# Performance work log

Measured on AMD Instinct MI355X. Metric: run time of the kernel, lower is better.

The kernel has to match this reference:

```python
import jax, jax.numpy as jnp
import numpy as np

H, NH, QLORA, KVLORA, DN, DR, DV = 2048, 16, 1536, 512, 128, 64, 128
QD = DN + DR  # 192
EPS = 1e-6
ROPE_BASE = 10000.0


def rmsnorm(x, g):
    var = jnp.mean(x * x, axis=-1, keepdims=True)
    return x * jax.lax.rsqrt(var + EPS) * g


def rotate_half(x):
    x1, x2 = jnp.split(x, 2, axis=-1)
    return jnp.concatenate([-x2, x1], axis=-1)


def rope_cos_sin(seq_len):
    inv_freq = 1.0 / (ROPE_BASE ** (jnp.arange(0, DR, 2, dtype=jnp.float32) / DR))
    t = jnp.arange(seq_len, dtype=jnp.float32)
    freqs = jnp.outer(t, inv_freq)           # [S, DR/2]
    emb = jnp.concatenate([freqs, freqs], -1)  # [S, DR]
    return jnp.cos(emb), jnp.sin(emb)


def setup_inputs() -> dict:
    key = jax.random.key(0)
    ks = jax.random.split(key, 6)
    B, S = 2, 2048
    sc = 0.02
    return {
        "hidden_states": jax.random.normal(ks[0], (B, S, H), jnp.float32),
        "w_qa": jax.random.normal(ks[1], (QLORA, H), jnp.float32) * sc,
        "g_qa": jnp.ones((QLORA,), jnp.float32),
        "w_qb": jax.random.normal(ks[2], (NH * QD, QLORA), jnp.float32) * sc,
        "w_kva": jax.random.normal(ks[3], (KVLORA + DR, H), jnp.float32) * sc,
        "g_kva": jnp.ones((KVLORA,), jnp.float32),
        "w_kvb": jax.random.normal(ks[4], (NH * (DN + DV), KVLORA), jnp.float32) * sc,
        "w_o": jax.random.normal(ks[5], (H, NH * DV), jnp.float32) * sc,
    }


def reference(hidden_states, w_qa, g_qa, w_qb, w_kva, g_kva, w_kvb, w_o):
    B, S, _ = hidden_states.shape
    # Q path: low-rank down-proj -> RMSNorm -> up-proj
    q_a = hidden_states @ w_qa.T                        # [B,S,QLORA]
    q = rmsnorm(q_a, g_qa) @ w_qb.T                     # [B,S,NH*QD]
    q = q.reshape(B, S, NH, QD).transpose(0, 2, 1, 3)   # [B,NH,S,QD]
    q_nope, q_pe = q[..., :DN], q[..., DN:]
    # KV path: joint down-proj with MQA rope slice
    ckv = hidden_states @ w_kva.T                       # [B,S,KVLORA+DR]
    compressed_kv, k_pe = ckv[..., :KVLORA], ckv[..., KVLORA:]
    k_pe = k_pe.reshape(B, S, 1, DR).transpose(0, 2, 1, 3)  # [B,1,S,DR]
    kv = rmsnorm(compressed_kv, g_kva) @ w_kvb.T        # [B,S,NH*(DN+DV)]
    kv = kv.reshape(B, S, NH, DN + DV).transpose(0, 2, 1, 3)
    k_nope, v = kv[..., :DN], kv[..., DN:]              # [B,NH,S,DN], [B,NH,S,DV]
    # decoupled RoPE on rope sub-dims only
    cos, sin = rope_cos_sin(S)                          # [S,DR]
    cos = cos[None, None]; sin = sin[None, None]
    q_pe = q_pe * cos + rotate_half(q_pe) * sin
    k_pe = k_pe * cos + rotate_half(k_pe) * sin
    query = jnp.concatenate([q_nope, q_pe], -1)         # [B,NH,S,QD]
    key = jnp.concatenate([k_nope, jnp.broadcast_to(k_pe, (B, NH, S, DR))], -1)
    # causal SDPA with scale = QD**-0.5
    scale = QD ** (-0.5)
    scores = jnp.einsum("bhsd,bhtd->bhst", query, key) * scale
    mask = jnp.tril(jnp.ones((S, S), bool))
    scores = jnp.where(mask, scores, jnp.finfo(scores.dtype).min)
    attn = jax.nn.softmax(scores, axis=-1)
    out = jnp.einsum("bhst,bhtd->bhsd", attn, v)        # [B,NH,S,DV]
    out = out.transpose(0, 2, 1, 3).reshape(B, S, NH * DV)
    return out @ w_o.T
```

## Files before the change

kernel.cpp:

```cpp
#include <hip/hip_runtime.h>
#include <cstdint>
#include <cstring>

typedef short short8 __attribute__((ext_vector_type(8)));
typedef float float4v __attribute__((ext_vector_type(4)));
typedef float float4g __attribute__((ext_vector_type(4)));
typedef unsigned short ushort4v __attribute__((ext_vector_type(4)));
typedef unsigned int uint2v __attribute__((ext_vector_type(2)));

typedef __attribute__((address_space(3))) unsigned int lds_uint;
typedef __attribute__((address_space(1))) const unsigned int glob_uint;

static __device__ __forceinline__ void async16(void* lds, const void* g) {
    __builtin_amdgcn_global_load_lds((glob_uint*)g, (lds_uint*)lds, 16, 0, 0);
}

static __device__ __forceinline__ float b2f(unsigned short u) {
    unsigned int x = ((unsigned int)u) << 16;
    float f;
    __builtin_memcpy(&f, &x, 4);
    return f;
}
static __device__ __forceinline__ unsigned short f2b(float f) {
    unsigned int x;
    __builtin_memcpy(&x, &f, 4);
    unsigned int r = (x + 0x7fffu + ((x >> 16) & 1u)) >> 16;
    return (unsigned short)r;
}

__global__ __launch_bounds__(256) void k_f2b6(
    const float* __restrict__ s0, unsigned short* __restrict__ d0,
    const float* __restrict__ s1, unsigned short* __restrict__ d1,
    const float* __restrict__ s2, unsigned short* __restrict__ d2,
    const float* __restrict__ s3, unsigned short* __restrict__ d3,
    const float* __restrict__ s4, unsigned short* __restrict__ d4,
    const float* __restrict__ s5, unsigned short* __restrict__ d5,
    float qs) {
    int blk = blockIdx.x;
    const float* s; unsigned short* d; float sc = 1.f; int rel;
    if (blk < 8192)       { s = s0; d = d0; rel = blk; }
    else if (blk < 11264) { s = s1; d = d1; rel = blk - 8192; }
    else if (blk < 15872) { s = s2; d = d2; rel = blk - 11264; sc = qs; }
    else if (blk < 17024) { s = s3; d = d3; rel = blk - 15872; }
    else if (blk < 19072) { s = s4; d = d4; rel = blk - 17024; }
    else                  { s = s5; d = d5; rel = blk - 19072; }
    int i = (rel * 256 + threadIdx.x) * 4;
    float4g v = *(const float4g*)(s + i);
    ushort4v r;
    r.x = f2b(v.x * sc); r.y = f2b(v.y * sc); r.z = f2b(v.z * sc); r.w = f2b(v.w * sc);
    *(ushort4v*)(d + i) = r;
}

static __device__ __forceinline__ void gemm_bt_body(
    const unsigned short* __restrict__ A, int lda,
    const unsigned short* __restrict__ W,
    void* __restrict__ C, int ldc,
    int N, int K, int c_fp32, int bx, int by) {
    __shared__ __align__(16) unsigned short As[128 * 32];
    __shared__ __align__(16) unsigned short Ws[128 * 32];
    const int tid = threadIdx.x;
    const int m0 = by * 128, n0 = bx * 128;
    const int wave = tid >> 6, lane = tid & 63;
    const int wm = (wave >> 1) * 64, wn = (wave & 1) * 64;
    const int lrow = lane & 15, quad = lane >> 4;
    const int srow = lane >> 2, spiece = lane & 3;

    float4v acc[4][4];
    float4v z = {0.f, 0.f, 0.f, 0.f};
#pragma unroll
    for (int i = 0; i < 4; i++)
#pragma unroll
        for (int j = 0; j < 4; j++) acc[i][j] = z;

    for (int k0 = 0; k0 < K; k0 += 32) {
#pragma unroll
        for (int ii = 0; ii < 2; ++ii) {
            int i = wave + ii * 4;
            int row = i * 16 + srow;
            async16(&As[i * 512], &A[(size_t)(m0 + row) * lda + k0 + spiece * 8]);
            int wr = n0 + row;
            if (wr > N - 1) wr = N - 1;
            async16(&Ws[i * 512], &W[(size_t)wr * K + k0 + spiece * 8]);
        }
        __syncthreads();
        short8 af[4], bfr[4];
#pragma unroll
        for (int i = 0; i < 4; i++)
            af[i] = *(const short8*)&As[(wm + i * 16 + lrow) * 32 + quad * 8];
#pragma unroll
        for (int i = 0; i < 4; i++)
            bfr[i] = *(const short8*)&Ws[(wn + i * 16 + lrow) * 32 + quad * 8];
#pragma unroll
        for (int i = 0; i < 4; i++)
#pragma unroll
            for (int j = 0; j < 4; j++)
                acc[i][j] = __builtin_amdgcn_mfma_f32_16x16x32_bf16(af[i], bfr[j], acc[i][j], 0, 0, 0);
        __syncthreads();
    }

    const int rbase = quad * 4;
#pragma unroll
    for (int i = 0; i < 4; i++) {
#pragma unroll
        for (int j = 0; j < 4; j++) {
            int col = n0 + wn + j * 16 + lrow;
            if (col >= N) continue;
#pragma unroll
            for (int r = 0; r < 4; r++) {
                int row = m0 + wm + i * 16 + rbase + r;
                float v = acc[i][j][r];
                if (c_fp32)
                    ((float*)C)[(size_t)row * ldc + col] = v;
                else
                    ((unsigned short*)C)[(size_t)row * ldc + col] = f2b(v);
            }
        }
    }
}

__global__ __launch_bounds__(256, 3)
void k_gemm_bt(const unsigned short* __restrict__ A, int lda,
               const unsigned short* __restrict__ W,
               void* __restrict__ C, int ldc,
               int N, int K, int c_fp32) {
    gemm_bt_body(A, lda, W, C, ldc, N, K, c_fp32, blockIdx.x, blockIdx.y);
}

__global__ __launch_bounds__(256, 3)
void k_gemm_dual(const unsigned short* __restrict__ A0, int lda0,
                 const unsigned short* __restrict__ W0, void* __restrict__ C0,
                 int ldc0, int N0, int K0, int nbx0,
                 const unsigned short* __restrict__ A1, int lda1,
                 const unsigned short* __restrict__ W1, void* __restrict__ C1,
                 int ldc1, int N1, int K1) {
    int bx = blockIdx.x;
    if (bx < nbx0) {
        gemm_bt_body(A0, lda0, W0, C0, ldc0, N0, K0, 0, bx, blockIdx.y);
    } else {
        gemm_bt_body(A1, lda1, W1, C1, ldc1, N1, K1, 0, bx - nbx0, blockIdx.y);
    }
}

__global__ void k_rmsnorm8(unsigned short* __restrict__ x, const float* __restrict__ g,
                           int ld, int n) {
    int row = blockIdx.x;
    int tid = threadIdx.x;
    size_t base = (size_t)row * ld + tid * 8;
    short8 v8 = *(const short8*)(x + base);
    float vf[8];
    float ss = 0.f;
#pragma unroll
    for (int i = 0; i < 8; i++) {
        vf[i] = b2f((unsigned short)v8[i]);
        ss += vf[i] * vf[i];
    }
    for (int off = 32; off > 0; off >>= 1) ss += __shfl_xor(ss, off);
    __shared__ float wsum[4];
    int nw = blockDim.x >> 6;
    if (nw > 1) {
        int wave = tid >> 6, lane = tid & 63;
        if (lane == 0) wsum[wave] = ss;
        __syncthreads();
        ss = 0.f;
        for (int w = 0; w < nw; w++) ss += wsum[w];
    }
    float scale = rsqrtf(ss / (float)n + 1e-6f);
    short8 r8;
#pragma unroll
    for (int i = 0; i < 8; i++) r8[i] = (short)f2b(vf[i] * scale * g[tid * 8 + i]);
    *(short8*)(x + base) = r8;
}

__global__ __launch_bounds__(256) void k_rope_q(unsigned short* __restrict__ q) {
    int idx = blockIdx.x * 256 + threadIdx.x;
    int d = idx & 31;
    int h = (idx >> 5) & 15;
    int t = idx >> 9;
    int s = t & 2047;
    size_t base = (size_t)t * 3072 + h * 192 + 128;
    float inv = exp2f((float)d * -0.4152410118609203f);
    float f = (float)s * inv;
    float c, sn;
    sincosf(f, &sn, &c);
    float x1 = b2f(q[base + d]), x2 = b2f(q[base + d + 32]);
    q[base + d] = f2b(x1 * c - x2 * sn);
    q[base + d + 32] = f2b(x2 * c + x1 * sn);
}

__global__ __launch_bounds__(256) void k_rope_k(unsigned short* __restrict__ ckv) {
    int idx = blockIdx.x * 256 + threadIdx.x;
    int d = idx & 31;
    int t = idx >> 5;
    int s = t & 2047;
    size_t base = (size_t)t * 576 + 512;
    float inv = exp2f((float)d * -0.4152410118609203f);
    float f = (float)s * inv;
    float c, sn;
    sincosf(f, &sn, &c);
    float x1 = b2f(ckv[base + d]), x2 = b2f(ckv[base + d + 32]);
    ckv[base + d] = f2b(x1 * c - x2 * sn);
    ckv[base + d + 32] = f2b(x2 * c + x1 * sn);
}

__global__ __launch_bounds__(256) void k_transpose_v(const unsigned short* __restrict__ kv,
                                                     unsigned short* __restrict__ vt) {
    int bh = blockIdx.z;
    int b = bh >> 4, h = bh & 15;
    int s0 = blockIdx.x * 32, d0 = blockIdx.y * 32;
    __shared__ unsigned short t[32][33];
    int tx = threadIdx.x & 31, ty = threadIdx.x >> 5;
#pragma unroll
    for (int i = 0; i < 4; i++) {
        int s = s0 + ty + i * 8;
        t[ty + i * 8][tx] = kv[(size_t)(b * 2048 + s) * 4096 + h * 256 + 128 + d0 + tx];
    }
    __syncthreads();
#pragma unroll
    for (int i = 0; i < 4; i++) {
        int d = d0 + ty + i * 8;
        vt[((size_t)bh * 128 + d) * 2048 + s0 + tx] = t[tx][ty + i * 8];
    }
}

__global__ __launch_bounds__(256, 2)
void k_attn6(const unsigned short* __restrict__ q,
             const unsigned short* __restrict__ kv,
             const unsigned short* __restrict__ ckv,
             const unsigned short* __restrict__ vt,
             unsigned short* __restrict__ ao)
{
    __shared__ __align__(16) unsigned short Ks[2][12288];
    __shared__ __align__(16) unsigned short Vs[8192];
    __shared__ __align__(16) unsigned short Pl[4][1280];

    const int lb = blockIdx.x;
    const int qt = (lb < 256) ? (lb >> 5) : 15 - ((lb & 255) >> 5);
    const int bh = lb & 31;
    const int b = bh >> 4, h = bh & 15;
    const int tid = threadIdx.x, wave = tid >> 6, lane = tid & 63;
    const int lrow = lane & 15, quad = lane >> 4;
    const int srow = lane >> 2, spiece = lane & 3;
    const int tok0 = b * 2048 + qt * 128;
    unsigned short* Pw = Pl[wave];

    const int colx = spiece ^ ((srow >> 1) & 3);
    const int qx = (quad ^ ((lrow >> 1) & 3)) * 8;

    short8 qf[2][6];
#pragma unroll
    for (int mi = 0; mi < 2; mi++) {
        const unsigned short* qp =
            q + (size_t)(tok0 + wave * 32 + mi * 16 + lrow) * 3072 + h * 192;
#pragma unroll
        for (int ks = 0; ks < 6; ks++) qf[mi][ks] = *(const short8*)(qp + ks * 32 + quad * 8);
    }

    short8 ones;
#pragma unroll
    for (int j = 0; j < 8; j++) ones[j] = (short)0x3F80;

    float m_st[2];
    m_st[0] = m_st[1] = -__builtin_inff();
    float4v z4 = {0.f, 0.f, 0.f, 0.f};
    float4v o[2][8], osum[2];
#pragma unroll
    for (int mi = 0; mi < 2; mi++) {
        osum[mi] = z4;
#pragma unroll
        for (int dt = 0; dt < 8; dt++) o[mi][dt] = z4;
    }

    const int nk = 2 * qt + 2;

    auto stageK = [&](int kt, int buf) {
        const int kb = kt * 64;
#pragma unroll
        for (int ii = 0; ii < 6; ++ii) {
            int id = wave * 6 + ii;
            int ks = id >> 2;
            int row = (id & 3) * 16 + srow;
            int key = b * 2048 + kb + row;
            const unsigned short* g =
                (ks < 4) ? kv + (size_t)key * 4096 + h * 256 + ks * 32 + colx * 8
                         : ckv + (size_t)key * 576 + 512 + (ks - 4) * 32 + colx * 8;
            async16(&Ks[buf][id * 512], g);
        }
    };
    auto stageV = [&](int kt) {
        const int kb = kt * 64;
#pragma unroll
        for (int ii = 0; ii < 4; ++ii) {
            int id = wave * 4 + ii;
            int d = (id & 7) * 16 + srow;
            const unsigned short* g =
                vt + ((size_t)bh * 128 + d) * 2048 + kb + (id >> 3) * 32 + colx * 8;
            async16(&Vs[id * 512], g);
        }
    };

    stageK(0, 0);

    for (int kt = 0; kt < nk; ++kt) {
        __syncthreads();
        stageV(kt);
        if (kt + 1 < nk) stageK(kt + 1, (kt + 1) & 1);
        const unsigned short* Kb = Ks[kt & 1];
        const int kb = kt * 64;

        float4v sc[2][4];
#pragma unroll
        for (int mi = 0; mi < 2; mi++)
#pragma unroll
            for (int nt = 0; nt < 4; nt++) sc[mi][nt] = z4;
        __builtin_amdgcn_s_setprio(1);
#pragma unroll
        for (int ks = 0; ks < 6; ks++) {
#pragma unroll
            for (int nt = 0; nt < 4; nt++) {
                short8 kf = *(const short8*)&Kb[ks * 2048 + nt * 512 + lrow * 32 + qx];
                sc[0][nt] = __builtin_amdgcn_mfma_f32_16x16x32_bf16(kf, qf[0][ks], sc[0][nt], 0, 0, 0);
                sc[1][nt] = __builtin_amdgcn_mfma_f32_16x16x32_bf16(kf, qf[1][ks], sc[1][nt], 0, 0, 0);
            }
        }
        __builtin_amdgcn_s_setprio(0);

        if (kt >= nk - 2) {
#pragma unroll
            for (int mi = 0; mi < 2; mi++) {
                int rowc = qt * 128 + wave * 32 + mi * 16 + lrow;
#pragma unroll
                for (int nt = 0; nt < 4; nt++)
#pragma unroll
                    for (int r = 0; r < 4; r++) {
                        int keyc = kb + nt * 16 + quad * 4 + r;
                        if (keyc > rowc) sc[mi][nt][r] = -__builtin_inff();
                    }
            }
        }

        float alpha[2];
        uint2v pk[2][4];
#pragma unroll
        for (int mi = 0; mi < 2; mi++) {
            float mx = sc[mi][0][0];
#pragma unroll
            for (int nt = 0; nt < 4; nt++)
#pragma unroll
                for (int r = 0; r < 4; r++) mx = fmaxf(mx, sc[mi][nt][r]);
            mx = fmaxf(mx, __shfl_xor(mx, 16));
            mx = fmaxf(mx, __shfl_xor(mx, 32));
            float mnew = fmaxf(m_st[mi], mx);
            alpha[mi] = exp2f(m_st[mi] - mnew);
            m_st[mi] = mnew;
#pragma unroll
            for (int nt = 0; nt < 4; nt++) {
                float p0 = exp2f(sc[mi][nt][0] - mnew);
                float p1 = exp2f(sc[mi][nt][1] - mnew);
                float p2 = exp2f(sc[mi][nt][2] - mnew);
                float p3 = exp2f(sc[mi][nt][3] - mnew);
                pk[mi][nt].x = (unsigned int)f2b(p0) | ((unsigned int)f2b(p1) << 16);
                pk[mi][nt].y = (unsigned int)f2b(p2) | ((unsigned int)f2b(p3) << 16);
            }
        }

        float arow[2][4];
#pragma unroll
        for (int mi = 0; mi < 2; mi++)
#pragma unroll
            for (int r = 0; r < 4; r++) arow[mi][r] = __shfl(alpha[mi], quad * 4 + r);
#pragma unroll
        for (int mi = 0; mi < 2; mi++) {
#pragma unroll
            for (int r = 0; r < 4; r++) osum[mi][r] *= arow[mi][r];
#pragma unroll
            for (int dt = 0; dt < 8; dt++)
#pragma unroll
                for (int r = 0; r < 4; r++) o[mi][dt][r] *= arow[mi][r];
        }

        __syncthreads();

#pragma unroll
        for (int ks2 = 0; ks2 < 2; ks2++) {
#pragma unroll
            for (int mi = 0; mi < 2; mi++) {
                int row = mi * 16 + lrow;
                *(uint2v*)&Pw[row * 40 + quad * 4] = pk[mi][ks2 * 2];
                *(uint2v*)&Pw[row * 40 + 16 + quad * 4] = pk[mi][ks2 * 2 + 1];
            }
            short8 pa0 = *(const short8*)&Pw[lrow * 40 + quad * 8];
            short8 pa1 = *(const short8*)&Pw[(16 + lrow) * 40 + quad * 8];
            __builtin_amdgcn_s_setprio(1);
#pragma unroll
            for (int dt = 0; dt < 8; dt++) {
                short8 vf = *(const short8*)&Vs[(ks2 * 8 + dt) * 512 + lrow * 32 + qx];
                o[0][dt] = __builtin_amdgcn_mfma_f32_16x16x32_bf16(pa0, vf, o[0][dt], 0, 0, 0);
                o[1][dt] = __builtin_amdgcn_mfma_f32_16x16x32_bf16(pa1, vf, o[1][dt], 0, 0, 0);
            }
            osum[0] = __builtin_amdgcn_mfma_f32_16x16x32_bf16(pa0, ones, osum[0], 0, 0, 0);
            osum[1] = __builtin_amdgcn_mfma_f32_16x16x32_bf16(pa1, ones, osum[1], 0, 0, 0);
            __builtin_amdgcn_s_setprio(0);
        }
    }

#pragma unroll
    for (int mi = 0; mi < 2; mi++) {
#pragma unroll
        for (int r = 0; r < 4; r++) {
            float linv = 1.f / osum[mi][r];
            unsigned short* dst =
                ao + (size_t)(tok0 + wave * 32 + mi * 16 + quad * 4 + r) * 2048 + h * 128;
#pragma unroll
            for (int dt = 0; dt < 8; dt++) dst[dt * 16 + lrow] = f2b(o[mi][dt][r] * linv);
        }
    }
}

extern "C" void kernel_launch(void* const* d_in, const int* in_sizes, int n_in,
                              void* d_out, int out_size, void* d_ws, size_t ws_size,
                              hipStream_t stream) {
    (void)in_sizes; (void)n_in; (void)out_size; (void)ws_size;
    const float* hs    = (const float*)d_in[0];
    const float* w_qa  = (const float*)d_in[1];
    const float* g_qa  = (const float*)d_in[2];
    const float* w_qb  = (const float*)d_in[3];
    const float* w_kva = (const float*)d_in[4];
    const float* g_kva = (const float*)d_in[5];
    const float* w_kvb = (const float*)d_in[6];
    const float* w_o   = (const float*)d_in[7];

    char* ws = (char*)d_ws;
    size_t off = 0;
    auto alloc = [&](size_t bytes) -> unsigned short* {
        unsigned short* p = (unsigned short*)(ws + off);
        off += (bytes + 255) & ~(size_t)255;
        return p;
    };
    unsigned short* hb    = alloc(4096ull * 2048 * 2);
    unsigned short* wqa   = alloc(1536ull * 2048 * 2);
    unsigned short* wqb   = alloc(3072ull * 1536 * 2);
    unsigned short* wkva  = alloc(576ull * 2048 * 2);
    unsigned short* wkvb  = alloc(4096ull * 512 * 2);
    unsigned short* wo    = alloc(2048ull * 2048 * 2);
    unsigned short* qa    = alloc(4096ull * 1536 * 2);
    unsigned short* ckv   = alloc(4096ull * 576 * 2);
    unsigned short* qbuf  = alloc(4096ull * 3072 * 2);
    unsigned short* kvbuf = alloc(4096ull * 4096 * 2);
    unsigned short* vtb   = alloc(32ull * 128 * 2048 * 2);
    unsigned short* ao    = alloc(4096ull * 2048 * 2);

    const float qscale = 0.07216878364870323f * 1.4426950408889634f;

    k_f2b6<<<dim3(23168), dim3(256), 0, stream>>>(
        hs, hb, w_qa, wqa, w_qb, wqb, w_kva, wkva, w_kvb, wkvb, w_o, wo, qscale);

    k_gemm_dual<<<dim3(17, 32), 256, 0, stream>>>(
        hb, 2048, wqa, qa, 1536, 1536, 2048, 12,
        hb, 2048, wkva, ckv, 576, 576, 2048);

    k_rmsnorm8<<<dim3(4096), dim3(192), 0, stream>>>(qa, g_qa, 1536, 1536);
    k_rmsnorm8<<<dim3(4096), dim3(64), 0, stream>>>(ckv, g_kva, 576, 512);
    k_rope_k<<<dim3(512), 256, 0, stream>>>(ckv);

    k_gemm_dual<<<dim3(56, 32), 256, 0, stream>>>(
        qa, 1536, wqb, qbuf, 3072, 3072, 1536, 24,
        ckv, 576, wkvb, kvbuf, 4096, 4096, 512);

    k_rope_q<<<dim3(8192), 256, 0, stream>>>(qbuf);
    k_transpose_v<<<dim3(64, 4, 32), 256, 0, stream>>>(kvbuf, vtb);
    k_attn6<<<dim3(512), 256, 0, stream>>>(qbuf, kvbuf, ckv, vtb, ao);
    k_gemm_bt<<<dim3(16, 32), 256, 0, stream>>>(ao, 2048, wo, d_out, 2048, 2048, 2048, 1);
}
```

Baseline: 445.1 us.

## Fuse norms and RoPE, pair causal tiles per block, double-buffer V, lazy rescale

The two RMSNorm launches and the K-side RoPE are merged into one kernel, and the Q-side RoPE now runs in the attention kernel's Q fragment load. Each attention block processes a complementary pair of causal query tiles (qt and 15-qt) for balanced work, launching 256 blocks with 1 block per CU. V is double-buffered alongside K, which removes one barrier per iteration. Online-softmax rescaling is skipped when the row max grows by at most 6 (log2 units). This cuts launches and memory passes, but halving the grid and occupancy may expose latency, and the lazy max threshold could in principle affect precision.

```diff
diff --git a/kernel.cpp b/kernel.cpp
--- a/kernel.cpp
+++ b/kernel.cpp
@@ -141,65 +141,63 @@
     }
 }
 
-__global__ void k_rmsnorm8(unsigned short* __restrict__ x, const float* __restrict__ g,
-                           int ld, int n) {
-    int row = blockIdx.x;
+__global__ __launch_bounds__(192) void k_norm2(
+    unsigned short* __restrict__ qa, const float* __restrict__ g_qa,
+    unsigned short* __restrict__ ckv, const float* __restrict__ g_kva) {
+    __shared__ float wsum[3];
+    int blk = blockIdx.x;
     int tid = threadIdx.x;
-    size_t base = (size_t)row * ld + tid * 8;
-    short8 v8 = *(const short8*)(x + base);
-    float vf[8];
-    float ss = 0.f;
-#pragma unroll
-    for (int i = 0; i < 8; i++) {
-        vf[i] = b2f((unsigned short)v8[i]);
-        ss += vf[i] * vf[i];
-    }
-    for (int off = 32; off > 0; off >>= 1) ss += __shfl_xor(ss, off);
-    __shared__ float wsum[4];
-    int nw = blockDim.x >> 6;
-    if (nw > 1) {
+    if (blk < 4096) {
+        size_t base = (size_t)blk * 1536 + tid * 8;
+        short8 v8 = *(const short8*)(qa + base);
+        float vf[8];
+        float ss = 0.f;
+#pragma unroll
+        for (int i = 0; i < 8; i++) {
+            vf[i] = b2f((unsigned short)v8[i]);
+            ss += vf[i] * vf[i];
+        }
+        for (int off = 32; off > 0; off >>= 1) ss += __shfl_xor(ss, off);
         int wave = tid >> 6, lane = tid & 63;
         if (lane == 0) wsum[wave] = ss;
         __syncthreads();
-        ss = 0.f;
-        for (int w = 0; w < nw; w++) ss += wsum[w];
-    }
-    float scale = rsqrtf(ss / (float)n + 1e-6f);
-    short8 r8;
-#pragma unroll
-    for (int i = 0; i < 8; i++) r8[i] = (short)f2b(vf[i] * scale * g[tid * 8 + i]);
-    *(short8*)(x + base) = r8;
-}
-
-__global__ __launch_bounds__(256) void k_rope_q(unsigned short* __restrict__ q) {
-    int idx = blockIdx.x * 256 + threadIdx.x;
-    int d = idx & 31;
-    int h = (idx >> 5) & 15;
-    int t = idx >> 9;
-    int s = t & 2047;
-    size_t base = (size_t)t * 3072 + h * 192 + 128;
-    float inv = exp2f((float)d * -0.4152410118609203f);
-    float f = (float)s * inv;
-    float c, sn;
-    sincosf(f, &sn, &c);
-    float x1 = b2f(q[base + d]), x2 = b2f(q[base + d + 32]);
-    q[base + d] = f2b(x1 * c - x2 * sn);
-    q[base + d + 32] = f2b(x2 * c + x1 * sn);
-}
-
-__global__ __launch_bounds__(256) void k_rope_k(unsigned short* __restrict__ ckv) {
-    int idx = blockIdx.x * 256 + threadIdx.x;
-    int d = idx & 31;
-    int t = idx >> 5;
-    int s = t & 2047;
-    size_t base = (size_t)t * 576 + 512;
-    float inv = exp2f((float)d * -0.4152410118609203f);
-    float f = (float)s * inv;
-    float c, sn;
-    sincosf(f, &sn, &c);
-    float x1 = b2f(ckv[base + d]), x2 = b2f(ckv[base + d + 32]);
-    ckv[base + d] = f2b(x1 * c - x2 * sn);
-    ckv[base + d + 32] = f2b(x2 * c + x1 * sn);
+        ss = wsum[0] + wsum[1] + wsum[2];
+        float scale = rsqrtf(ss * (1.f / 1536.f) + 1e-6f);
+        short8 r8;
+#pragma unroll
+        for (int i = 0; i < 8; i++) r8[i] = (short)f2b(vf[i] * scale * g_qa[tid * 8 + i]);
+        *(short8*)(qa + base) = r8;
+    } else {
+        int row = blk - 4096;
+        if (tid < 64) {
+            size_t base = (size_t)row * 576 + tid * 8;
+            short8 v8 = *(const short8*)(ckv + base);
+            float vf[8];
+            float ss = 0.f;
+#pragma unroll
+            for (int i = 0; i < 8; i++) {
+                vf[i] = b2f((unsigned short)v8[i]);
+                ss += vf[i] * vf[i];
+            }
+            for (int off = 32; off > 0; off >>= 1) ss += __shfl_xor(ss, off);
+            float scale = rsqrtf(ss * (1.f / 512.f) + 1e-6f);
+            short8 r8;
+#pragma unroll
+            for (int i = 0; i < 8; i++) r8[i] = (short)f2b(vf[i] * scale * g_kva[tid * 8 + i]);
+            *(short8*)(ckv + base) = r8;
+        } else if (tid < 96) {
+            int d = tid - 64;
+            int s = row & 2047;
+            size_t base = (size_t)row * 576 + 512;
+            float inv = exp2f((float)d * -0.4152410118609203f);
+            float f = (float)s * inv;
+            float c, sn;
+            sincosf(f, &sn, &c);
+            float x1 = b2f(ckv[base + d]), x2 = b2f(ckv[base + d + 32]);
+            ckv[base + d] = f2b(x1 * c - x2 * sn);
+            ckv[base + d + 32] = f2b(x2 * c + x1 * sn);
+        }
+    }
 }
 
 __global__ __launch_bounds__(256) void k_transpose_v(const unsigned short* __restrict__ kv,
@@ -222,55 +220,38 @@
     }
 }
 
-__global__ __launch_bounds__(256, 2)
-void k_attn6(const unsigned short* __restrict__ q,
+__global__ __launch_bounds__(256, 1)
+void k_attn8(const unsigned short* __restrict__ q,
              const unsigned short* __restrict__ kv,
              const unsigned short* __restrict__ ckv,
              const unsigned short* __restrict__ vt,
              unsigned short* __restrict__ ao)
 {
     __shared__ __align__(16) unsigned short Ks[2][12288];
-    __shared__ __align__(16) unsigned short Vs[8192];
+    __shared__ __align__(16) unsigned short Vs[2][8192];
     __shared__ __align__(16) unsigned short Pl[4][1280];
 
-    const int lb = blockIdx.x;
-    const int qt = (lb < 256) ? (lb >> 5) : 15 - ((lb & 255) >> 5);
-    const int bh = lb & 31;
+    const int pb = blockIdx.x >> 5;
+    const int bh = blockIdx.x & 31;
     const int b = bh >> 4, h = bh & 15;
     const int tid = threadIdx.x, wave = tid >> 6, lane = tid & 63;
     const int lrow = lane & 15, quad = lane >> 4;
     const int srow = lane >> 2, spiece = lane & 3;
-    const int tok0 = b * 2048 + qt * 128;
     unsigned short* Pw = Pl[wave];
 
     const int colx = spiece ^ ((srow >> 1) & 3);
     const int qx = (quad ^ ((lrow >> 1) & 3)) * 8;
 
-    short8 qf[2][6];
-#pragma unroll
-    for (int mi = 0; mi < 2; mi++) {
-        const unsigned short* qp =
-            q + (size_t)(tok0 + wave * 32 + mi * 16 + lrow) * 3072 + h * 192;
-#pragma unroll
-        for (int ks = 0; ks < 6; ks++) qf[mi][ks] = *(const short8*)(qp + ks * 32 + quad * 8);
-    }
+    float invf[8];
+#pragma unroll
+    for (int j = 0; j < 8; j++)
+        invf[j] = exp2f((float)(quad * 8 + j) * -0.4152410118609203f);
 
     short8 ones;
 #pragma unroll
     for (int j = 0; j < 8; j++) ones[j] = (short)0x3F80;
 
-    float m_st[2];
-    m_st[0] = m_st[1] = -__builtin_inff();
     float4v z4 = {0.f, 0.f, 0.f, 0.f};
-    float4v o[2][8], osum[2];
-#pragma unroll
-    for (int mi = 0; mi < 2; mi++) {
-        osum[mi] = z4;
-#pragma unroll
-        for (int dt = 0; dt < 8; dt++) o[mi][dt] = z4;
-    }
-
-    const int nk = 2 * qt + 2;
 
     auto stageK = [&](int kt, int buf) {
         const int kb = kt * 64;
@@ -286,7 +267,7 @@
             async16(&Ks[buf][id * 512], g);
         }
     };
-    auto stageV = [&](int kt) {
+    auto stageV = [&](int kt, int buf) {
         const int kb = kt * 64;
 #pragma unroll
         for (int ii = 0; ii < 4; ++ii) {
@@ -294,124 +275,173 @@
             int d = (id & 7) * 16 + srow;
             const unsigned short* g =
                 vt + ((size_t)bh * 128 + d) * 2048 + kb + (id >> 3) * 32 + colx * 8;
-            async16(&Vs[id * 512], g);
+            async16(&Vs[buf][id * 512], g);
         }
     };
 
-    stageK(0, 0);
-
-    for (int kt = 0; kt < nk; ++kt) {
+    for (int pass = 0; pass < 2; ++pass) {
+        const int qt = pass ? (15 - pb) : pb;
+        const int tok0 = b * 2048 + qt * 128;
+        const int nk = 2 * qt + 2;
+
+        short8 qf[2][6];
+#pragma unroll
+        for (int mi = 0; mi < 2; mi++) {
+            int row = wave * 32 + mi * 16 + lrow;
+            const unsigned short* qp = q + (size_t)(tok0 + row) * 3072 + h * 192;
+#pragma unroll
+            for (int ks = 0; ks < 6; ks++) qf[mi][ks] = *(const short8*)(qp + ks * 32 + quad * 8);
+            float sp = (float)(qt * 128 + row);
+#pragma unroll
+            for (int j = 0; j < 8; j++) {
+                float f = sp * invf[j];
+                float c, sn;
+                sincosf(f, &sn, &c);
+                float x1 = b2f((unsigned short)qf[mi][4][j]);
+                float x2 = b2f((unsigned short)qf[mi][5][j]);
+                qf[mi][4][j] = (short)f2b(x1 * c - x2 * sn);
+                qf[mi][5][j] = (short)f2b(x2 * c + x1 * sn);
+            }
+        }
+
+        float m_st[2];
+        m_st[0] = m_st[1] = -__builtin_inff();
+        float4v o[2][8], osum[2];
+#pragma unroll
+        for (int mi = 0; mi < 2; mi++) {
+            osum[mi] = z4;
+#pragma unroll
+            for (int dt = 0; dt < 8; dt++) o[mi][dt] = z4;
+        }
+
         __syncthreads();
-        stageV(kt);
-        if (kt + 1 < nk) stageK(kt + 1, (kt + 1) & 1);
-        const unsigned short* Kb = Ks[kt & 1];
-        const int kb = kt * 64;
-
-        float4v sc[2][4];
-#pragma unroll
-        for (int mi = 0; mi < 2; mi++)
-#pragma unroll
-            for (int nt = 0; nt < 4; nt++) sc[mi][nt] = z4;
-        __builtin_amdgcn_s_setprio(1);
-#pragma unroll
-        for (int ks = 0; ks < 6; ks++) {
-#pragma unroll
-            for (int nt = 0; nt < 4; nt++) {
-                short8 kf = *(const short8*)&Kb[ks * 2048 + nt * 512 + lrow * 32 + qx];
-                sc[0][nt] = __builtin_amdgcn_mfma_f32_16x16x32_bf16(kf, qf[0][ks], sc[0][nt], 0, 0, 0);
-                sc[1][nt] = __builtin_amdgcn_mfma_f32_16x16x32_bf16(kf, qf[1][ks], sc[1][nt], 0, 0, 0);
-            }
-        }
-        __builtin_amdgcn_s_setprio(0);
-
-        if (kt >= nk - 2) {
+        stageK(0, 0);
+        stageV(0, 0);
+
+        for (int kt = 0; kt < nk; ++kt) {
+            __syncthreads();
+            if (kt + 1 < nk) {
+                stageK(kt + 1, (kt + 1) & 1);
+                stageV(kt + 1, (kt + 1) & 1);
+            }
+            const unsigned short* Kb = Ks[kt & 1];
+            const unsigned short* Vb = Vs[kt & 1];
+            const int kb = kt * 64;
+
+            float4v sc[2][4];
+#pragma unroll
+            for (int mi = 0; mi < 2; mi++)
+#pragma unroll
+                for (int nt = 0; nt < 4; nt++) sc[mi][nt] = z4;
+            __builtin_amdgcn_s_setprio(1);
+#pragma unroll
+            for (int ks = 0; ks < 6; ks++) {
+#pragma unroll
+                for (int nt = 0; nt < 4; nt++) {
+                    short8 kf = *(const short8*)&Kb[ks * 2048 + nt * 512 + lrow * 32 + qx];
+                    sc[0][nt] = __builtin_amdgcn_mfma_f32_16x16x32_bf16(kf, qf[0][ks], sc[0][nt], 0, 0, 0);
+                    sc[1][nt] = __builtin_amdgcn_mfma_f32_16x16x32_bf16(kf, qf[1][ks], sc[1][nt], 0, 0, 0);
+                }
+            }
+            __builtin_amdgcn_s_setprio(0);
+
+            if (kt >= nk - 2) {
+#pragma unroll
+                for (int mi = 0; mi < 2; mi++) {
+                    int rowc = qt * 128 + wave * 32 + mi * 16 + lrow;
+#pragma unroll
+                    for (int nt = 0; nt < 4; nt++)
+#pragma unroll
+                        for (int r = 0; r < 4; r++) {
+                            int keyc = kb + nt * 16 + quad * 4 + r;
+                            if (keyc > rowc) sc[mi][nt][r] = -__builtin_inff();
+                        }
+                }
+            }
+
+            float mx[2];
 #pragma unroll
             for (int mi = 0; mi < 2; mi++) {
-                int rowc = qt * 128 + wave * 32 + mi * 16 + lrow;
+                float m = sc[mi][0][0];
 #pragma unroll
                 for (int nt = 0; nt < 4; nt++)
 #pragma unroll
-                    for (int r = 0; r < 4; r++) {
-                        int keyc = kb + nt * 16 + quad * 4 + r;
-                        if (keyc > rowc) sc[mi][nt][r] = -__builtin_inff();
-                    }
-            }
-        }
-
-        float alpha[2];
-        uint2v pk[2][4];
+                    for (int r = 0; r < 4; r++) m = fmaxf(m, sc[mi][nt][r]);
+                m = fmaxf(m, __shfl_xor(m, 16));
+                m = fmaxf(m, __shfl_xor(m, 32));
+                mx[mi] = m;
+            }
+            bool within = (mx[0] <= m_st[0] + 6.f) && (mx[1] <= m_st[1] + 6.f);
+            if (!__all(within)) {
+                float alpha[2];
+#pragma unroll
+                for (int mi = 0; mi < 2; mi++) {
+                    float mnew = fmaxf(m_st[mi], mx[mi]);
+                    alpha[mi] = exp2f(m_st[mi] - mnew);
+                    m_st[mi] = mnew;
+                }
+                float arow[2][4];
+#pragma unroll
+                for (int mi = 0; mi < 2; mi++)
+#pragma unroll
+                    for (int r = 0; r < 4; r++) arow[mi][r] = __shfl(alpha[mi], quad * 4 + r);
+#pragma unroll
+                for (int mi = 0; mi < 2; mi++) {
+#pragma unroll
+                    for (int r = 0; r < 4; r++) osum[mi][r] *= arow[mi][r];
+#pragma unroll
+                    for (int dt = 0; dt < 8; dt++)
+#pragma unroll
+                        for (int r = 0; r < 4; r++) o[mi][dt][r] *= arow[mi][r];
+                }
+            }
+            uint2v pk[2][4];
+#pragma unroll
+            for (int mi = 0; mi < 2; mi++) {
+#pragma unroll
+                for (int nt = 0; nt < 4; nt++) {
+                    float p0 = exp2f(sc[mi][nt][0] - m_st[mi]);
+                    float p1 = exp2f(sc[mi][nt][1] - m_st[mi]);
+                    float p2 = exp2f(sc[mi][nt][2] - m_st[mi]);
+                    float p3 = exp2f(sc[mi][nt][3] - m_st[mi]);
+                    pk[mi][nt].x = (unsigned int)f2b(p0) | ((unsigned int)f2b(p1) << 16);
+                    pk[mi][nt].y = (unsigned int)f2b(p2) | ((unsigned int)f2b(p3) << 16);
+                }
+            }
+
+#pragma unroll
+            for (int ks2 = 0; ks2 < 2; ks2++) {
+#pragma unroll
+                for (int mi = 0; mi < 2; mi++) {
+                    int row = mi * 16 + lrow;
+                    *(uint2v*)&Pw[row * 40 + quad * 4] = pk[mi][ks2 * 2];
+                    *(uint2v*)&Pw[row * 40 + 16 + quad * 4] = pk[mi][ks2 * 2 + 1];
+                }
+                short8 pa0 = *(const short8*)&Pw[lrow * 40 + quad * 8];
+                short8 pa1 = *(const short8*)&Pw[(16 + lrow) * 40 + quad * 8];
+                __builtin_amdgcn_s_setprio(1);
+#pragma unroll
+                for (int dt = 0; dt < 8; dt++) {
+                    short8 vf = *(const short8*)&Vb[(ks2 * 8 + dt) * 512 + lrow * 32 + qx];
+                    o[0][dt] = __builtin_amdgcn_mfma_f32_16x16x32_bf16(pa0, vf, o[0][dt], 0, 0, 0);
+                    o[1][dt] = __builtin_amdgcn_mfma_f32_16x16x32_bf16(pa1, vf, o[1][dt], 0, 0, 0);
+                }
+                osum[0] = __builtin_amdgcn_mfma_f32_16x16x32_bf16(pa0, ones, osum[0], 0, 0, 0);
+                osum[1] = __builtin_amdgcn_mfma_f32_16x16x32_bf16(pa1, ones, osum[1], 0, 0, 0);
+                __builtin_amdgcn_s_setprio(0);
+            }
+        }
+
 #pragma unroll
         for (int mi = 0; mi < 2; mi++) {
-            float mx = sc[mi][0][0];
-#pragma unroll
-            for (int nt = 0; nt < 4; nt++)
-#pragma unroll
-                for (int r = 0; r < 4; r++) mx = fmaxf(mx, sc[mi][nt][r]);
-            mx = fmaxf(mx, __shfl_xor(mx, 16));
-            mx = fmaxf(mx, __shfl_xor(mx, 32));
-            float mnew = fmaxf(m_st[mi], mx);
-            alpha[mi] = exp2f(m_st[mi] - mnew);
-            m_st[mi] = mnew;
-#pragma unroll
-            for (int nt = 0; nt < 4; nt++) {
-                float p0 = exp2f(sc[mi][nt][0] - mnew);
-                float p1 = exp2f(sc[mi][nt][1] - mnew);
-                float p2 = exp2f(sc[mi][nt][2] - mnew);
-                float p3 = exp2f(sc[mi][nt][3] - mnew);
-                pk[mi][nt].x = (unsigned int)f2b(p0) | ((unsigned int)f2b(p1) << 16);
-                pk[mi][nt].y = (unsigned int)f2b(p2) | ((unsigned int)f2b(p3) << 16);
-            }
-        }
-
-        float arow[2][4];
-#pragma unroll
-        for (int mi = 0; mi < 2; mi++)
-#pragma unroll
-            for (int r = 0; r < 4; r++) arow[mi][r] = __shfl(alpha[mi], quad * 4 + r);
-#pragma unroll
-        for (int mi = 0; mi < 2; mi++) {
-#pragma unroll
-            for (int r = 0; r < 4; r++) osum[mi][r] *= arow[mi][r];
-#pragma unroll
-            for (int dt = 0; dt < 8; dt++)
-#pragma unroll
-                for (int r = 0; r < 4; r++) o[mi][dt][r] *= arow[mi][r];
-        }
-
-        __syncthreads();
-
-#pragma unroll
-        for (int ks2 = 0; ks2 < 2; ks2++) {
-#pragma unroll
-            for (int mi = 0; mi < 2; mi++) {
-                int row = mi * 16 + lrow;
-                *(uint2v*)&Pw[row * 40 + quad * 4] = pk[mi][ks2 * 2];
-                *(uint2v*)&Pw[row * 40 + 16 + quad * 4] = pk[mi][ks2 * 2 + 1];
-            }
-            short8 pa0 = *(const short8*)&Pw[lrow * 40 + quad * 8];
-            short8 pa1 = *(const short8*)&Pw[(16 + lrow) * 40 + quad * 8];
-            __builtin_amdgcn_s_setprio(1);
-#pragma unroll
-            for (int dt = 0; dt < 8; dt++) {
-                short8 vf = *(const short8*)&Vs[(ks2 * 8 + dt) * 512 + lrow * 32 + qx];
-                o[0][dt] = __builtin_amdgcn_mfma_f32_16x16x32_bf16(pa0, vf, o[0][dt], 0, 0, 0);
-                o[1][dt] = __builtin_amdgcn_mfma_f32_16x16x32_bf16(pa1, vf, o[1][dt], 0, 0, 0);
-            }
-            osum[0] = __builtin_amdgcn_mfma_f32_16x16x32_bf16(pa0, ones, osum[0], 0, 0, 0);
-            osum[1] = __builtin_amdgcn_mfma_f32_16x16x32_bf16(pa1, ones, osum[1], 0, 0, 0);
-            __builtin_amdgcn_s_setprio(0);
-        }
-    }
-
-#pragma unroll
-    for (int mi = 0; mi < 2; mi++) {
-#pragma unroll
-        for (int r = 0; r < 4; r++) {
-            float linv = 1.f / osum[mi][r];
-            unsigned short* dst =
-                ao + (size_t)(tok0 + wave * 32 + mi * 16 + quad * 4 + r) * 2048 + h * 128;
-#pragma unroll
-            for (int dt = 0; dt < 8; dt++) dst[dt * 16 + lrow] = f2b(o[mi][dt][r] * linv);
+#pragma unroll
+            for (int r = 0; r < 4; r++) {
+                float linv = 1.f / osum[mi][r];
+                unsigned short* dst =
+                    ao + (size_t)(tok0 + wave * 32 + mi * 16 + quad * 4 + r) * 2048 + h * 128;
+#pragma unroll
+                for (int dt = 0; dt < 8; dt++) dst[dt * 16 + lrow] = f2b(o[mi][dt][r] * linv);
+            }
         }
     }
 }
@@ -458,16 +488,13 @@
         hb, 2048, wqa, qa, 1536, 1536, 2048, 12,
         hb, 2048, wkva, ckv, 576, 576, 2048);
 
-    k_rmsnorm8<<<dim3(4096), dim3(192), 0, stream>>>(qa, g_qa, 1536, 1536);
-    k_rmsnorm8<<<dim3(4096), dim3(64), 0, stream>>>(ckv, g_kva, 576, 512);
-    k_rope_k<<<dim3(512), 256, 0, stream>>>(ckv);
+    k_norm2<<<dim3(8192), dim3(192), 0, stream>>>(qa, g_qa, ckv, g_kva);
 
     k_gemm_dual<<<dim3(56, 32), 256, 0, stream>>>(
         qa, 1536, wqb, qbuf, 3072, 3072, 1536, 24,
         ckv, 576, wkvb, kvbuf, 4096, 4096, 512);
 
-    k_rope_q<<<dim3(8192), 256, 0, stream>>>(qbuf);
     k_transpose_v<<<dim3(64, 4, 32), 256, 0, stream>>>(kvbuf, vtb);
-    k_attn6<<<dim3(512), 256, 0, stream>>>(qbuf, kvbuf, ckv, vtb, ao);
+    k_attn8<<<dim3(256), 256, 0, stream>>>(qbuf, kvbuf, ckv, vtb, ao);
     k_gemm_bt<<<dim3(16, 32), 256, 0, stream>>>(ao, 2048, wo, d_out, 2048, 2048, 2048, 1);
 }
```

After: 452.8 us. No clear change (+1.7%).
